# Performance work log

Measured on AMD Instinct MI355X. Metric: run time of the kernel, lower is better.

The kernel has to match this reference:

```python
import jax, jax.numpy as jnp
import numpy as np

B, S, H = 2, 2048, 2048
N = 16               # num heads
NOPE, ROPE, V = 128, 64, 128
QHD = NOPE + ROPE    # 192 per-head q/k dim
QL, KVL = 1536, 512  # q_lora_rank, kv_lora_rank
THETA = 10000.0
SCALE = QHD ** -0.5
EPS = 1e-6


def rmsnorm(x, w):
    var = jnp.mean(x.astype(jnp.float32) ** 2, axis=-1, keepdims=True)
    return (x.astype(jnp.float32) * jax.lax.rsqrt(var + EPS)).astype(x.dtype) * w


def rotate_half(x):
    d = x.shape[-1] // 2
    return jnp.concatenate([-x[..., d:], x[..., :d]], axis=-1)


def setup_inputs() -> dict:
    key = jax.random.key(0)
    ks = jax.random.split(key, 8)
    w = lambda k, shape: jax.random.normal(k, shape, jnp.float32) * 0.02
    return {
        "hidden_states": jax.random.normal(ks[0], (B, S, H), jnp.float32),
        "position_ids": (jnp.arange(B * S, dtype=jnp.int64) % 4096).reshape(B, S),
        "q_a_w": w(ks[1], (QL, H)),
        "q_a_ln_w": jnp.ones((QL,), jnp.float32),
        "q_b_w": w(ks[2], (N * QHD, QL)),
        "kv_a_w": w(ks[3], (KVL + ROPE, H)),
        "kv_a_ln_w": jnp.ones((KVL,), jnp.float32),
        "kv_b_w": w(ks[4], (N * (NOPE + V), KVL)),
        "o_w": w(ks[5], (H, N * V)),
    }


def mla_forward(hidden_states, position_ids, q_a_w, q_a_ln_w, q_b_w,
                kv_a_w, kv_a_ln_w, kv_b_w, o_w):
    b, s, _ = hidden_states.shape
    # ---- Q low-rank path: q_b(rmsnorm(q_a(x))) ----
    q = rmsnorm(hidden_states @ q_a_w.T, q_a_ln_w) @ q_b_w.T
    q = q.reshape(b, s, N, QHD)
    q_nope, q_pe = q[..., :NOPE], q[..., NOPE:]
    # ---- compressed KV + shared rope key ----
    kv_a = hidden_states @ kv_a_w.T                       # [b,s,KVL+ROPE]
    compressed_kv = rmsnorm(kv_a[..., :KVL], kv_a_ln_w)   # [b,s,KVL]
    k_pe = kv_a[..., KVL:].reshape(b, s, 1, ROPE)         # MQA rope key
    # ---- RoPE (default, theta=1e4) from position_ids ----
    inv_freq = 1.0 / (THETA ** (jnp.arange(0, ROPE, 2, dtype=jnp.float32) / ROPE))
    freqs = position_ids.astype(jnp.float32)[..., None] * inv_freq  # [b,s,ROPE/2]
    emb = jnp.concatenate([freqs, freqs], axis=-1)                  # [b,s,ROPE]
    cos = jnp.cos(emb)[:, :, None, :].astype(hidden_states.dtype)   # [b,s,1,ROPE]
    sin = jnp.sin(emb)[:, :, None, :].astype(hidden_states.dtype)
    q_pe = q_pe * cos + rotate_half(q_pe) * sin
    k_pe = k_pe * cos + rotate_half(k_pe) * sin
    # ---- decompress latent KV via kv_b_proj ----
    kv = (compressed_kv @ kv_b_w.T).reshape(b, s, N, NOPE + V)
    k_nope, v = kv[..., :NOPE], kv[..., NOPE:]
    k = jnp.concatenate([k_nope, jnp.broadcast_to(k_pe, (b, s, N, ROPE))], axis=-1)
    qf = jnp.concatenate([q_nope, q_pe], axis=-1)          # [b,s,N,QHD]
    # ---- causal SDPA in bsnd layout ----
    scores = jnp.einsum('bqnd,bknd->bnqk', qf, k) * SCALE  # [b,N,s,s]
    causal = jnp.tril(jnp.ones((s, s), bool))
    scores = jnp.where(causal, scores, jnp.finfo(scores.dtype).min)
    probs = jax.nn.softmax(scores, axis=-1)
    attn = jnp.einsum('bnqk,bknd->bqnd', probs, v)         # [b,s,N,V]
    out = attn.reshape(b, s, N * V) @ o_w.T
    return out


def reference(hidden_states, position_ids, q_a_w, q_a_ln_w, q_b_w,
              kv_a_w, kv_a_ln_w, kv_b_w, o_w):
    return mla_forward(hidden_states, position_ids, q_a_w, q_a_ln_w, q_b_w,
                       kv_a_w, kv_a_ln_w, kv_b_w, o_w)
```

## Files before the change

kernel.cpp:

```cpp
#include <hip/hip_runtime.h>
#include <cstdio>

typedef unsigned short u16;
typedef u16 u16x4 __attribute__((ext_vector_type(4)));
typedef u16 u16x8 __attribute__((ext_vector_type(8)));
typedef __bf16 bf16x8 __attribute__((ext_vector_type(8)));
typedef float f32x4 __attribute__((ext_vector_type(4)));

#define AS1 __attribute__((address_space(1)))
#define AS3 __attribute__((address_space(3)))

#define GLOAD16(gsrc, ldst) __builtin_amdgcn_global_load_lds( \
    (const AS1 void*)(gsrc), (AS3 void*)(ldst), 16, 0, 0)

__device__ __forceinline__ u16 f2bf(float f) {
  unsigned u = __builtin_bit_cast(unsigned, f);
  u += 0x7fffu + ((u >> 16) & 1u);
  return (u16)(u >> 16);
}
__device__ __forceinline__ float bf2f(u16 h) {
  return __builtin_bit_cast(float, (unsigned)h << 16);
}

__global__ __launch_bounds__(256) void cvt_pad_k(const float* __restrict__ src,
                                                 u16* __restrict__ dst,
                                                 long srcN, long dstN) {
  long i = ((long)blockIdx.x * 256 + threadIdx.x) * 8;
  const long stride = (long)gridDim.x * 256 * 8;
  for (; i < dstN; i += stride) {
    u16x8 o = {0,0,0,0,0,0,0,0};
    if (i < srcN) {
      const float4* p = (const float4*)(src + i);
      float4 a = p[0], b = p[1];
      o[0]=f2bf(a.x); o[1]=f2bf(a.y); o[2]=f2bf(a.z); o[3]=f2bf(a.w);
      o[4]=f2bf(b.x); o[5]=f2bf(b.y); o[6]=f2bf(b.z); o[7]=f2bf(b.w);
    }
    *(u16x8*)(dst + i) = o;
  }
}

__global__ __launch_bounds__(256) void rms_k(const u16* __restrict__ src, u16* __restrict__ dst,
                                             const float* __restrict__ w,
                                             int sstride, int dstride, int cols) {
  const int row = blockIdx.x;
  const int tid = threadIdx.x;
  const int nch = cols >> 3;
  float x[8];
  float ss = 0.f;
  if (tid < nch) {
    u16x8 v = *(const u16x8*)(src + (size_t)row * sstride + tid * 8);
#pragma unroll
    for (int j = 0; j < 8; ++j) { x[j] = bf2f(v[j]); ss += x[j] * x[j]; }
  } else {
#pragma unroll
    for (int j = 0; j < 8; ++j) x[j] = 0.f;
  }
#pragma unroll
  for (int off = 1; off < 64; off <<= 1) ss += __shfl_xor(ss, off);
  __shared__ float red[4];
  const int wv = tid >> 6, ln = tid & 63;
  if (ln == 0) red[wv] = ss;
  __syncthreads();
  const float tot = red[0] + red[1] + red[2] + red[3];
  const float rs = 1.0f / sqrtf(tot / (float)cols + 1e-6f);
  if (tid < nch) {
    u16x8 o;
#pragma unroll
    for (int j = 0; j < 8; ++j) o[j] = f2bf(x[j] * rs * w[tid * 8 + j]);
    *(u16x8*)(dst + (size_t)row * dstride + tid * 8) = o;
  }
}

__global__ __launch_bounds__(256) void rope_k(u16* __restrict__ q, const u16* __restrict__ kva,
                                              u16* __restrict__ kpe, const int* __restrict__ pos) {
  const int tok = blockIdx.x;
  const int j = threadIdx.x & 63;
  const int w = threadIdx.x >> 6;
  const float p = (float)pos[tok];
  const int jj = j & 31;
  const float inv = __powf(10000.0f, -(float)jj * (1.0f / 32.0f));
  float s, c;
  __sincosf(p * inv, &s, &c);
  const float sgn = (j < 32) ? -1.0f : 1.0f;
  const int partner = (j < 32) ? j + 32 : j - 32;
  if (w == 0) {
    const float x  = bf2f(kva[(size_t)tok * 640 + 512 + j]);
    const float xp = bf2f(kva[(size_t)tok * 640 + 512 + partner]);
    kpe[(size_t)tok * 64 + j] = f2bf(x * c + sgn * xp * s);
  }
#pragma unroll
  for (int hh = 0; hh < 4; ++hh) {
    const int h = w * 4 + hh;
    const size_t base = (size_t)tok * 3072 + h * 192 + 128;
    const float x  = bf2f(q[base + j]);
    const float xp = bf2f(q[base + partner]);
    q[base + j] = f2bf(x * c + sgn * xp * s);
  }
}

__global__ __launch_bounds__(256) void gemm_bt(const u16* __restrict__ A, const u16* __restrict__ B,
                                               u16* __restrict__ Cb, float* __restrict__ Cf,
                                               int M, int N, int K) {
  __shared__ __attribute__((aligned(16))) u16 As[128 * 64];
  __shared__ __attribute__((aligned(16))) u16 Bs[128 * 64];
  const int tid = threadIdx.x;
  const int m0 = blockIdx.y * 128, n0 = blockIdx.x * 128;
  const int w = tid >> 6, lane = tid & 63;
  const int wr = w >> 1, wc = w & 1;
  const int lr = lane & 15, g = lane >> 4;

  f32x4 acc[4][4] = {};

  for (int k0 = 0; k0 < K; k0 += 64) {
#pragma unroll
    for (int i = 0; i < 4; ++i) {
      const int c = i * 256 + tid;
      const int row = c >> 3, col = (c & 7) << 3;
      GLOAD16(A + (size_t)(m0 + row) * K + k0 + col, &As[c * 8]);
    }
#pragma unroll
    for (int i = 0; i < 4; ++i) {
      const int c = i * 256 + tid;
      const int row = c >> 3, col = (c & 7) << 3;
      GLOAD16(B + (size_t)(n0 + row) * K + k0 + col, &Bs[c * 8]);
    }
    __syncthreads();
    bf16x8 af[4][2], bfr[4][2];
#pragma unroll
    for (int x = 0; x < 4; ++x)
#pragma unroll
      for (int kk = 0; kk < 2; ++kk) {
        af[x][kk]  = *(const bf16x8*)(&As[(wr * 64 + x * 16 + lr) * 64 + kk * 32 + g * 8]);
        bfr[x][kk] = *(const bf16x8*)(&Bs[(wc * 64 + x * 16 + lr) * 64 + kk * 32 + g * 8]);
      }
#pragma unroll
    for (int mi = 0; mi < 4; ++mi)
#pragma unroll
      for (int ni = 0; ni < 4; ++ni)
#pragma unroll
        for (int kk = 0; kk < 2; ++kk)
          acc[mi][ni] = __builtin_amdgcn_mfma_f32_16x16x32_bf16(af[mi][kk], bfr[ni][kk],
                                                                acc[mi][ni], 0, 0, 0);
    __syncthreads();
  }

  const int rb = m0 + wr * 64, cb = n0 + wc * 64;
#pragma unroll
  for (int mi = 0; mi < 4; ++mi)
#pragma unroll
    for (int ni = 0; ni < 4; ++ni)
#pragma unroll
      for (int i = 0; i < 4; ++i) {
        const int r = rb + mi * 16 + g * 4 + i;
        const int cI = cb + ni * 16 + lr;
        if (Cf) Cf[(size_t)r * N + cI] = acc[mi][ni][i];
        else    Cb[(size_t)r * N + cI] = f2bf(acc[mi][ni][i]);
      }
}

__global__ __launch_bounds__(256) void attn_k(const u16* __restrict__ q, const u16* __restrict__ kvb,
                                              const u16* __restrict__ kpe, u16* __restrict__ ao) {
  __shared__ __attribute__((aligned(16))) u16 Ks[64 * 192];
  __shared__ __attribute__((aligned(16))) u16 Vt[128 * 64];

  const float SCALE = 0.07216878364870323f;
  const int bh = blockIdx.x;
  const int b = bh >> 4, h = bh & 15;
  const int j = 15 - blockIdx.y;
  const int tid = threadIdx.x, w = tid >> 6, lane = tid & 63;
  const int lr = lane & 15, g = lane >> 4;

  const int q0 = j * 128;
  const int qrb = q0 + w * 32;
  u16* Psw = &Ks[w * 2304];

  bf16x8 qf[2][6];
#pragma unroll
  for (int m = 0; m < 2; ++m)
#pragma unroll
    for (int kd = 0; kd < 6; ++kd)
      qf[m][kd] = *(const bf16x8*)(q + (size_t)(b * 2048 + qrb + m * 16 + lr) * 3072 +
                                   h * 192 + kd * 32 + g * 8);

  float mrow[2][4], lrow[2][4];
  f32x4 o[2][8] = {};
#pragma unroll
  for (int m = 0; m < 2; ++m)
#pragma unroll
    for (int i = 0; i < 4; ++i) { mrow[m][i] = -1e30f; lrow[m][i] = 0.f; }

  const int nt = (q0 >> 6) + 2;
  for (int t = 0; t < nt; ++t) {
    const int k0 = t * 64;
#pragma unroll
    for (int i = 0; i < 6; ++i) {
      const int c = i * 256 + tid;
      const int row = c / 24, cl = c - row * 24;
      const int cg = cl ^ (row & 7);
      const u16* src = (cg < 16)
        ? (kvb + (size_t)(b * 2048 + k0 + row) * 4096 + h * 256 + cg * 8)
        : (kpe + (size_t)(b * 2048 + k0 + row) * 64 + (cg - 16) * 8);
      GLOAD16(src, &Ks[c * 8]);
    }
    {
      const int kq = tid >> 4;
      const int vc = (tid & 15) << 3;
      u16x8 vv[4];
#pragma unroll
      for (int r = 0; r < 4; ++r)
        vv[r] = *(const u16x8*)(kvb + (size_t)(b * 2048 + k0 + kq * 4 + r) * 4096 + h * 256 + 128 + vc);
#pragma unroll
      for (int e = 0; e < 8; ++e) {
        const int v = vc + e;
        const int cx = (kq >> 1) ^ (v & 7) ^ ((v >> 3) & 7);
        u16x4 tq = {vv[0][e], vv[1][e], vv[2][e], vv[3][e]};
        *(u16x4*)(&Vt[v * 64 + cx * 8 + (kq & 1) * 4]) = tq;
      }
    }
    __syncthreads();

    const bool active = (k0 <= qrb + 31);
    f32x4 sAcc[2][4] = {};
    if (active) {
#pragma unroll
      for (int nf = 0; nf < 4; ++nf) {
        const int rr = nf * 16 + lr;
#pragma unroll
        for (int kd = 0; kd < 6; ++kd) {
          const int ch = (kd * 4 + g) ^ (rr & 7);
          const bf16x8 kf = *(const bf16x8*)(&Ks[rr * 192 + ch * 8]);
#pragma unroll
          for (int m = 0; m < 2; ++m)
            sAcc[m][nf] = __builtin_amdgcn_mfma_f32_16x16x32_bf16(qf[m][kd], kf, sAcc[m][nf], 0, 0, 0);
        }
      }
    }
    __syncthreads();

    if (active) {
#pragma unroll
      for (int m = 0; m < 2; ++m) {
        float sv[4][4];
#pragma unroll
        for (int nf = 0; nf < 4; ++nf)
#pragma unroll
          for (int i = 0; i < 4; ++i) {
            const int qrow = qrb + m * 16 + g * 4 + i;
            const int kcol = k0 + nf * 16 + lr;
            const float vS = sAcc[m][nf][i] * SCALE;
            sv[nf][i] = (kcol > qrow) ? -1e30f : vS;
          }
        float fac[4], mn[4];
#pragma unroll
        for (int i = 0; i < 4; ++i) {
          float rm = fmaxf(fmaxf(sv[0][i], sv[1][i]), fmaxf(sv[2][i], sv[3][i]));
          rm = fmaxf(rm, __shfl_xor(rm, 1));
          rm = fmaxf(rm, __shfl_xor(rm, 2));
          rm = fmaxf(rm, __shfl_xor(rm, 4));
          rm = fmaxf(rm, __shfl_xor(rm, 8));
          mn[i] = fmaxf(mrow[m][i], rm);
          fac[i] = __expf(mrow[m][i] - mn[i]);
          mrow[m][i] = mn[i];
        }
#pragma unroll
        for (int i = 0; i < 4; ++i) {
          float rsum = 0.f;
#pragma unroll
          for (int nf = 0; nf < 4; ++nf) { sv[nf][i] = __expf(sv[nf][i] - mn[i]); rsum += sv[nf][i]; }
          rsum += __shfl_xor(rsum, 1);
          rsum += __shfl_xor(rsum, 2);
          rsum += __shfl_xor(rsum, 4);
          rsum += __shfl_xor(rsum, 8);
          lrow[m][i] = lrow[m][i] * fac[i] + rsum;
        }
#pragma unroll
        for (int nv = 0; nv < 8; ++nv)
#pragma unroll
          for (int i = 0; i < 4; ++i) o[m][nv][i] *= fac[i];
#pragma unroll
        for (int nf = 0; nf < 4; ++nf)
#pragma unroll
          for (int i = 0; i < 4; ++i)
            Psw[(m * 16 + g * 4 + i) * 72 + nf * 16 + lr] = f2bf(sv[nf][i]);
      }
      asm volatile("s_waitcnt lgkmcnt(0)" ::: "memory");

#pragma unroll
      for (int kc = 0; kc < 2; ++kc) {
        bf16x8 vfr[8];
#pragma unroll
        for (int nv = 0; nv < 8; ++nv) {
          const int v = nv * 16 + lr;
          const int cx = (kc * 4 + g) ^ (v & 7) ^ ((v >> 3) & 7);
          vfr[nv] = *(const bf16x8*)(&Vt[v * 64 + cx * 8]);
        }
#pragma unroll
        for (int m = 0; m < 2; ++m) {
          const bf16x8 pf = *(const bf16x8*)(&Psw[(m * 16 + lr) * 72 + kc * 32 + g * 8]);
#pragma unroll
          for (int nv = 0; nv < 8; ++nv)
            o[m][nv] = __builtin_amdgcn_mfma_f32_16x16x32_bf16(pf, vfr[nv], o[m][nv], 0, 0, 0);
        }
      }
    }
    __syncthreads();
  }

#pragma unroll
  for (int m = 0; m < 2; ++m)
#pragma unroll
    for (int i = 0; i < 4; ++i) {
      const float inv = 1.0f / lrow[m][i];
      const size_t tokOff = (size_t)(b * 2048 + qrb + m * 16 + g * 4 + i) * 2048 + h * 128;
#pragma unroll
      for (int nv = 0; nv < 8; ++nv)
        ao[tokOff + nv * 16 + lr] = f2bf(o[m][nv][i] * inv);
    }
}

extern "C" void kernel_launch(void* const* d_in, const int* in_sizes, int n_in,
                              void* d_out, int out_size, void* d_ws, size_t ws_size,
                              hipStream_t stream) {
  const float* hidden  = (const float*)d_in[0];
  const int*   pos     = (const int*)d_in[1];
  const float* q_a_w   = (const float*)d_in[2];
  const float* q_a_ln  = (const float*)d_in[3];
  const float* q_b_w   = (const float*)d_in[4];
  const float* kv_a_w  = (const float*)d_in[5];
  const float* kv_a_ln = (const float*)d_in[6];
  const float* kv_b_w  = (const float*)d_in[7];
  const float* o_w     = (const float*)d_in[8];
  float* out = (float*)d_out;

  char* ws = (char*)d_ws;
  u16* hb  = (u16*)(ws + 0L);
  u16* w1  = (u16*)(ws + 16777216L);
  u16* w2  = (u16*)(ws + 23068672L);
  u16* w3  = (u16*)(ws + 32505856L);
  u16* w4  = (u16*)(ws + 35127296L);
  u16* w5  = (u16*)(ws + 39321600L);
  u16* qa  = (u16*)(ws + 47710208L);
  u16* qb  = (u16*)(ws + 60293120L);
  u16* kva = (u16*)(ws + 85458944L);
  u16* ckv = (u16*)(ws + 90701824L);
  u16* kpe = (u16*)(ws + 94896128L);
  u16* kvb = (u16*)(ws + 95420416L);
  u16* ao  = (u16*)(ws + 128974848L);
  if (ws_size < 145752064UL) { fprintf(stderr, "ws too small: %zu\n", ws_size); return; }

  auto cvt = [&](const float* s, u16* d, long sn, long dn) {
    long blocks = (dn / 8 + 255) / 256; if (blocks > 2048) blocks = 2048;
    cvt_pad_k<<<dim3((unsigned)blocks), dim3(256), 0, stream>>>(s, d, sn, dn);
  };
  cvt(hidden, hb, 4096L * 2048, 4096L * 2048);
  cvt(q_a_w,  w1, 1536L * 2048, 1536L * 2048);
  cvt(q_b_w,  w2, 3072L * 1536, 3072L * 1536);
  cvt(kv_a_w, w3, 576L * 2048,  640L * 2048);
  cvt(kv_b_w, w4, 4096L * 512,  4096L * 512);
  cvt(o_w,    w5, 2048L * 2048, 2048L * 2048);

  gemm_bt<<<dim3(12, 32), 256, 0, stream>>>(hb, w1, qa, nullptr, 4096, 1536, 2048);
  rms_k<<<4096, 256, 0, stream>>>(qa, qa, q_a_ln, 1536, 1536, 1536);
  gemm_bt<<<dim3(24, 32), 256, 0, stream>>>(qa, w2, qb, nullptr, 4096, 3072, 1536);
  gemm_bt<<<dim3(5, 32), 256, 0, stream>>>(hb, w3, kva, nullptr, 4096, 640, 2048);
  rms_k<<<4096, 256, 0, stream>>>(kva, ckv, kv_a_ln, 640, 512, 512);
  rope_k<<<4096, 256, 0, stream>>>(qb, kva, kpe, pos);
  gemm_bt<<<dim3(32, 32), 256, 0, stream>>>(ckv, w4, kvb, nullptr, 4096, 4096, 512);
  attn_k<<<dim3(32, 16), 256, 0, stream>>>(qb, kvb, kpe, ao);
  gemm_bt<<<dim3(16, 32), 256, 0, stream>>>(ao, w5, nullptr, out, 4096, 2048, 2048);
}
```

Before: 474.1 us.

## Split attention query tile across 8 waves with 16 rows each

The attention kernel now runs 512 threads per block, so each of the 8 waves owns 16 query rows instead of 32, which halves per-wave accumulator and Q-fragment registers. K tile loads are spread over all 512 threads, the V transpose is done by the first 256, and the per-wave P scratch is resized to match. The aim is more waves in flight and better latency hiding. In exchange, each K/V fragment read from LDS now feeds half as many MFMAs, barriers cover more waves, and half the threads sit idle during the V transpose.

```diff
diff --git a/kernel.cpp b/kernel.cpp
--- a/kernel.cpp
+++ b/kernel.cpp
@@ -158,8 +158,8 @@
       }
 }
 
-__global__ __launch_bounds__(256) void attn_k(const u16* __restrict__ q, const u16* __restrict__ kvb,
-                                              const u16* __restrict__ kpe, u16* __restrict__ ao) {
+__global__ __launch_bounds__(512, 4) void attn_k(const u16* __restrict__ q, const u16* __restrict__ kvb,
+                                                 const u16* __restrict__ kpe, u16* __restrict__ ao) {
   __shared__ __attribute__((aligned(16))) u16 Ks[64 * 192];
   __shared__ __attribute__((aligned(16))) u16 Vt[128 * 64];
 
@@ -171,30 +171,26 @@
   const int lr = lane & 15, g = lane >> 4;
 
   const int q0 = j * 128;
-  const int qrb = q0 + w * 32;
-  u16* Psw = &Ks[w * 2304];
-
-  bf16x8 qf[2][6];
-#pragma unroll
-  for (int m = 0; m < 2; ++m)
-#pragma unroll
-    for (int kd = 0; kd < 6; ++kd)
-      qf[m][kd] = *(const bf16x8*)(q + (size_t)(b * 2048 + qrb + m * 16 + lr) * 3072 +
-                                   h * 192 + kd * 32 + g * 8);
-
-  float mrow[2][4], lrow[2][4];
-  f32x4 o[2][8] = {};
-#pragma unroll
-  for (int m = 0; m < 2; ++m)
-#pragma unroll
-    for (int i = 0; i < 4; ++i) { mrow[m][i] = -1e30f; lrow[m][i] = 0.f; }
+  const int qrb = q0 + w * 16;
+  u16* Psw = &Ks[w * 1152];
+
+  bf16x8 qf[6];
+#pragma unroll
+  for (int kd = 0; kd < 6; ++kd)
+    qf[kd] = *(const bf16x8*)(q + (size_t)(b * 2048 + qrb + lr) * 3072 +
+                              h * 192 + kd * 32 + g * 8);
+
+  float mrow[4], lrow[4];
+  f32x4 o[8] = {};
+#pragma unroll
+  for (int i = 0; i < 4; ++i) { mrow[i] = -1e30f; lrow[i] = 0.f; }
 
   const int nt = (q0 >> 6) + 2;
   for (int t = 0; t < nt; ++t) {
     const int k0 = t * 64;
 #pragma unroll
-    for (int i = 0; i < 6; ++i) {
-      const int c = i * 256 + tid;
+    for (int i = 0; i < 3; ++i) {
+      const int c = i * 512 + tid;
       const int row = c / 24, cl = c - row * 24;
       const int cg = cl ^ (row & 7);
       const u16* src = (cg < 16)
@@ -202,7 +198,7 @@
         : (kpe + (size_t)(b * 2048 + k0 + row) * 64 + (cg - 16) * 8);
       GLOAD16(src, &Ks[c * 8]);
     }
-    {
+    if (tid < 256) {
       const int kq = tid >> 4;
       const int vc = (tid & 15) << 3;
       u16x8 vv[4];
@@ -219,8 +215,8 @@
     }
     __syncthreads();
 
-    const bool active = (k0 <= qrb + 31);
-    f32x4 sAcc[2][4] = {};
+    const bool active = (k0 <= qrb + 15);
+    f32x4 sAcc[4] = {};
     if (active) {
 #pragma unroll
       for (int nf = 0; nf < 4; ++nf) {
@@ -229,60 +225,55 @@
         for (int kd = 0; kd < 6; ++kd) {
           const int ch = (kd * 4 + g) ^ (rr & 7);
           const bf16x8 kf = *(const bf16x8*)(&Ks[rr * 192 + ch * 8]);
-#pragma unroll
-          for (int m = 0; m < 2; ++m)
-            sAcc[m][nf] = __builtin_amdgcn_mfma_f32_16x16x32_bf16(qf[m][kd], kf, sAcc[m][nf], 0, 0, 0);
+          sAcc[nf] = __builtin_amdgcn_mfma_f32_16x16x32_bf16(qf[kd], kf, sAcc[nf], 0, 0, 0);
         }
       }
     }
     __syncthreads();
 
     if (active) {
-#pragma unroll
-      for (int m = 0; m < 2; ++m) {
-        float sv[4][4];
-#pragma unroll
-        for (int nf = 0; nf < 4; ++nf)
-#pragma unroll
-          for (int i = 0; i < 4; ++i) {
-            const int qrow = qrb + m * 16 + g * 4 + i;
-            const int kcol = k0 + nf * 16 + lr;
-            const float vS = sAcc[m][nf][i] * SCALE;
-            sv[nf][i] = (kcol > qrow) ? -1e30f : vS;
-          }
-        float fac[4], mn[4];
+      float sv[4][4];
+#pragma unroll
+      for (int nf = 0; nf < 4; ++nf)
 #pragma unroll
         for (int i = 0; i < 4; ++i) {
-          float rm = fmaxf(fmaxf(sv[0][i], sv[1][i]), fmaxf(sv[2][i], sv[3][i]));
-          rm = fmaxf(rm, __shfl_xor(rm, 1));
-          rm = fmaxf(rm, __shfl_xor(rm, 2));
-          rm = fmaxf(rm, __shfl_xor(rm, 4));
-          rm = fmaxf(rm, __shfl_xor(rm, 8));
-          mn[i] = fmaxf(mrow[m][i], rm);
-          fac[i] = __expf(mrow[m][i] - mn[i]);
-          mrow[m][i] = mn[i];
+          const int qrow = qrb + g * 4 + i;
+          const int kcol = k0 + nf * 16 + lr;
+          const float vS = sAcc[nf][i] * SCALE;
+          sv[nf][i] = (kcol > qrow) ? -1e30f : vS;
         }
-#pragma unroll
-        for (int i = 0; i < 4; ++i) {
-          float rsum = 0.f;
-#pragma unroll
-          for (int nf = 0; nf < 4; ++nf) { sv[nf][i] = __expf(sv[nf][i] - mn[i]); rsum += sv[nf][i]; }
-          rsum += __shfl_xor(rsum, 1);
-          rsum += __shfl_xor(rsum, 2);
-          rsum += __shfl_xor(rsum, 4);
-          rsum += __shfl_xor(rsum, 8);
-          lrow[m][i] = lrow[m][i] * fac[i] + rsum;
-        }
-#pragma unroll
-        for (int nv = 0; nv < 8; ++nv)
-#pragma unroll
-          for (int i = 0; i < 4; ++i) o[m][nv][i] *= fac[i];
-#pragma unroll
-        for (int nf = 0; nf < 4; ++nf)
-#pragma unroll
-          for (int i = 0; i < 4; ++i)
-            Psw[(m * 16 + g * 4 + i) * 72 + nf * 16 + lr] = f2bf(sv[nf][i]);
-      }
+      float fac[4], mn[4];
+#pragma unroll
+      for (int i = 0; i < 4; ++i) {
+        float rm = fmaxf(fmaxf(sv[0][i], sv[1][i]), fmaxf(sv[2][i], sv[3][i]));
+        rm = fmaxf(rm, __shfl_xor(rm, 1));
+        rm = fmaxf(rm, __shfl_xor(rm, 2));
+        rm = fmaxf(rm, __shfl_xor(rm, 4));
+        rm = fmaxf(rm, __shfl_xor(rm, 8));
+        mn[i] = fmaxf(mrow[i], rm);
+        fac[i] = __expf(mrow[i] - mn[i]);
+        mrow[i] = mn[i];
+      }
+#pragma unroll
+      for (int i = 0; i < 4; ++i) {
+        float rsum = 0.f;
+#pragma unroll
+        for (int nf = 0; nf < 4; ++nf) { sv[nf][i] = __expf(sv[nf][i] - mn[i]); rsum += sv[nf][i]; }
+        rsum += __shfl_xor(rsum, 1);
+        rsum += __shfl_xor(rsum, 2);
+        rsum += __shfl_xor(rsum, 4);
+        rsum += __shfl_xor(rsum, 8);
+        lrow[i] = lrow[i] * fac[i] + rsum;
+      }
+#pragma unroll
+      for (int nv = 0; nv < 8; ++nv)
+#pragma unroll
+        for (int i = 0; i < 4; ++i) o[nv][i] *= fac[i];
+#pragma unroll
+      for (int nf = 0; nf < 4; ++nf)
+#pragma unroll
+        for (int i = 0; i < 4; ++i)
+          Psw[(g * 4 + i) * 72 + nf * 16 + lr] = f2bf(sv[nf][i]);
       asm volatile("s_waitcnt lgkmcnt(0)" ::: "memory");
 
 #pragma unroll
@@ -294,28 +285,23 @@
           const int cx = (kc * 4 + g) ^ (v & 7) ^ ((v >> 3) & 7);
           vfr[nv] = *(const bf16x8*)(&Vt[v * 64 + cx * 8]);
         }
-#pragma unroll
-        for (int m = 0; m < 2; ++m) {
-          const bf16x8 pf = *(const bf16x8*)(&Psw[(m * 16 + lr) * 72 + kc * 32 + g * 8]);
-#pragma unroll
-          for (int nv = 0; nv < 8; ++nv)
-            o[m][nv] = __builtin_amdgcn_mfma_f32_16x16x32_bf16(pf, vfr[nv], o[m][nv], 0, 0, 0);
-        }
-      }
-    }
-    __syncthreads();
-  }
-
-#pragma unroll
-  for (int m = 0; m < 2; ++m)
-#pragma unroll
-    for (int i = 0; i < 4; ++i) {
-      const float inv = 1.0f / lrow[m][i];
-      const size_t tokOff = (size_t)(b * 2048 + qrb + m * 16 + g * 4 + i) * 2048 + h * 128;
-#pragma unroll
-      for (int nv = 0; nv < 8; ++nv)
-        ao[tokOff + nv * 16 + lr] = f2bf(o[m][nv][i] * inv);
-    }
+        const bf16x8 pf = *(const bf16x8*)(&Psw[lr * 72 + kc * 32 + g * 8]);
+#pragma unroll
+        for (int nv = 0; nv < 8; ++nv)
+          o[nv] = __builtin_amdgcn_mfma_f32_16x16x32_bf16(pf, vfr[nv], o[nv], 0, 0, 0);
+      }
+    }
+    __syncthreads();
+  }
+
+#pragma unroll
+  for (int i = 0; i < 4; ++i) {
+    const float inv = 1.0f / lrow[i];
+    const size_t tokOff = (size_t)(b * 2048 + qrb + g * 4 + i) * 2048 + h * 128;
+#pragma unroll
+    for (int nv = 0; nv < 8; ++nv)
+      ao[tokOff + nv * 16 + lr] = f2bf(o[nv][i] * inv);
+  }
 }
 
 extern "C" void kernel_launch(void* const* d_in, const int* in_sizes, int n_in,
@@ -366,6 +352,6 @@
   rms_k<<<4096, 256, 0, stream>>>(kva, ckv, kv_a_ln, 640, 512, 512);
   rope_k<<<4096, 256, 0, stream>>>(qb, kva, kpe, pos);
   gemm_bt<<<dim3(32, 32), 256, 0, stream>>>(ckv, w4, kvb, nullptr, 4096, 4096, 512);
-  attn_k<<<dim3(32, 16), 256, 0, stream>>>(qb, kvb, kpe, ao);
+  attn_k<<<dim3(32, 16), 512, 0, stream>>>(qb, kvb, kpe, ao);
   gemm_bt<<<dim3(16, 32), 256, 0, stream>>>(ao, w5, nullptr, out, 4096, 2048, 2048);
 }
```

New measurement: 485.5 us. 1.02x slower.

## Pre-transpose V into a separate buffer and load it asynchronously in attention

Applied to the files above, without the earlier changes.

Adds a kernel that transposes the V part of the decompressed KV into a per-head [V, seq] layout, stored in the reused hidden-state buffer. The attention kernel then fills its V tile with direct global-to-LDS loads using a simpler XOR swizzle, replacing the register gather and scatter transpose done inside each tile iteration. This removes per-tile transpose work and its stalls from the attention loop. In exchange it adds an extra launch and a full read and write of V through global memory.

```diff
diff --git a/kernel.cpp b/kernel.cpp
--- a/kernel.cpp
+++ b/kernel.cpp
@@ -2,7 +2,6 @@
 #include <cstdio>
 
 typedef unsigned short u16;
-typedef u16 u16x4 __attribute__((ext_vector_type(4)));
 typedef u16 u16x8 __attribute__((ext_vector_type(8)));
 typedef __bf16 bf16x8 __attribute__((ext_vector_type(8)));
 typedef float f32x4 __attribute__((ext_vector_type(4)));
@@ -158,8 +157,37 @@
       }
 }
 
+__global__ __launch_bounds__(256) void vtr_k(const u16* __restrict__ kvb, u16* __restrict__ vT) {
+  __shared__ u16 tile[128 * 72];
+  const int bh = blockIdx.x, b = bh >> 4, h = bh & 15;
+  const int s0 = blockIdx.y * 64;
+  const int t = threadIdx.x;
+  {
+    const int s = t >> 2;
+    const int vc = (t & 3) * 32;
+    const u16* src = kvb + (size_t)(b * 2048 + s0 + s) * 4096 + h * 256 + 128 + vc;
+#pragma unroll
+    for (int c = 0; c < 4; ++c) {
+      u16x8 v = *(const u16x8*)(src + c * 8);
+#pragma unroll
+      for (int e = 0; e < 8; ++e) tile[(vc + c * 8 + e) * 72 + s] = v[e];
+    }
+  }
+  __syncthreads();
+  {
+    const int v = t >> 1;
+    const int sh = (t & 1) * 32;
+    u16* dst = vT + (size_t)(bh * 128 + v) * 2048 + s0 + sh;
+    const u16* srow = &tile[v * 72 + sh];
+#pragma unroll
+    for (int c = 0; c < 4; ++c)
+      *(u16x8*)(dst + c * 8) = *(const u16x8*)(srow + c * 8);
+  }
+}
+
 __global__ __launch_bounds__(256) void attn_k(const u16* __restrict__ q, const u16* __restrict__ kvb,
-                                              const u16* __restrict__ kpe, u16* __restrict__ ao) {
+                                              const u16* __restrict__ kpe, const u16* __restrict__ vT,
+                                              u16* __restrict__ ao) {
   __shared__ __attribute__((aligned(16))) u16 Ks[64 * 192];
   __shared__ __attribute__((aligned(16))) u16 Vt[128 * 64];
 
@@ -202,20 +230,12 @@
         : (kpe + (size_t)(b * 2048 + k0 + row) * 64 + (cg - 16) * 8);
       GLOAD16(src, &Ks[c * 8]);
     }
-    {
-      const int kq = tid >> 4;
-      const int vc = (tid & 15) << 3;
-      u16x8 vv[4];
-#pragma unroll
-      for (int r = 0; r < 4; ++r)
-        vv[r] = *(const u16x8*)(kvb + (size_t)(b * 2048 + k0 + kq * 4 + r) * 4096 + h * 256 + 128 + vc);
-#pragma unroll
-      for (int e = 0; e < 8; ++e) {
-        const int v = vc + e;
-        const int cx = (kq >> 1) ^ (v & 7) ^ ((v >> 3) & 7);
-        u16x4 tq = {vv[0][e], vv[1][e], vv[2][e], vv[3][e]};
-        *(u16x4*)(&Vt[v * 64 + cx * 8 + (kq & 1) * 4]) = tq;
-      }
+#pragma unroll
+    for (int i = 0; i < 4; ++i) {
+      const int c = i * 256 + tid;
+      const int v = c >> 3, cl = c & 7;
+      const int cg = cl ^ (v & 7);
+      GLOAD16(vT + (size_t)(bh * 128 + v) * 2048 + k0 + cg * 8, &Vt[c * 8]);
     }
     __syncthreads();
 
@@ -291,7 +311,7 @@
 #pragma unroll
         for (int nv = 0; nv < 8; ++nv) {
           const int v = nv * 16 + lr;
-          const int cx = (kc * 4 + g) ^ (v & 7) ^ ((v >> 3) & 7);
+          const int cx = (kc * 4 + g) ^ (v & 7);
           vfr[nv] = *(const bf16x8*)(&Vt[v * 64 + cx * 8]);
         }
 #pragma unroll
@@ -346,6 +366,7 @@
   u16* kpe = (u16*)(ws + 94896128L);
   u16* kvb = (u16*)(ws + 95420416L);
   u16* ao  = (u16*)(ws + 128974848L);
+  u16* vT  = hb;
   if (ws_size < 145752064UL) { fprintf(stderr, "ws too small: %zu\n", ws_size); return; }
 
   auto cvt = [&](const float* s, u16* d, long sn, long dn) {
@@ -366,6 +387,7 @@
   rms_k<<<4096, 256, 0, stream>>>(kva, ckv, kv_a_ln, 640, 512, 512);
   rope_k<<<4096, 256, 0, stream>>>(qb, kva, kpe, pos);
   gemm_bt<<<dim3(32, 32), 256, 0, stream>>>(ckv, w4, kvb, nullptr, 4096, 4096, 512);
-  attn_k<<<dim3(32, 16), 256, 0, stream>>>(qb, kvb, kpe, ao);
+  vtr_k<<<dim3(32, 32), 256, 0, stream>>>(kvb, vT);
+  attn_k<<<dim3(32, 16), 256, 0, stream>>>(qb, kvb, kpe, vT, ao);
   gemm_bt<<<dim3(16, 32), 256, 0, stream>>>(ao, w5, nullptr, out, 4096, 2048, 2048);
 }
```

Result: no change. 474.9 us (+0.2%).
